# Kernel optimization log

Hardware: AMD Instinct MI355X
Metric: run time of the kernel (lower is better)

Reference implementation:

```python
import jax, jax.numpy as jnp
from jax import lax
import numpy as np

V, D, H, CO = 50000, 300, 512, 100
B, S, W = 64, 32, 128


def setup_inputs() -> dict:
    key = jax.random.key(0)
    ks = jax.random.split(key, 24)
    sc = 0.1  # mimic uniform(-0.1, 0.1)-style small init; keeps tanh unsaturated
    inp = {
        "paragraphs": jax.random.randint(ks[0], (B, S, W), 0, V, dtype=jnp.int64),
        "embed_table": jax.random.normal(ks[1], (V, D), jnp.float32),
        "conv_w3": jax.random.normal(ks[2], (CO, 1, 3, D), jnp.float32) * 0.05,
        "conv_b3": jax.random.normal(ks[3], (CO,), jnp.float32) * sc,
        "conv_w4": jax.random.normal(ks[4], (CO, 1, 4, D), jnp.float32) * 0.05,
        "conv_b4": jax.random.normal(ks[5], (CO,), jnp.float32) * sc,
        "conv_w5": jax.random.normal(ks[6], (CO, 1, 5, D), jnp.float32) * 0.05,
        "conv_b5": jax.random.normal(ks[7], (CO,), jnp.float32) * sc,
        "proj_w": jax.random.normal(ks[8], (300, 300), jnp.float32) * sc,
        "proj_b": jax.random.normal(ks[9], (300,), jnp.float32) * sc,
        "init_w": jax.random.normal(ks[10], (H, 300), jnp.float32) * sc,
        "init_b": jax.random.normal(ks[11], (H,), jnp.float32) * sc,
        "w_ih_f": jax.random.normal(ks[12], (H, 300), jnp.float32) * sc,
        "w_hh_f": jax.random.normal(ks[13], (H, H), jnp.float32) * sc,
        "b_ih_f": jax.random.normal(ks[14], (H,), jnp.float32) * sc,
        "b_hh_f": jax.random.normal(ks[15], (H,), jnp.float32) * sc,
        "w_ih_b": jax.random.normal(ks[16], (H, 300), jnp.float32) * sc,
        "w_hh_b": jax.random.normal(ks[17], (H, H), jnp.float32) * sc,
        "b_ih_b": jax.random.normal(ks[18], (H,), jnp.float32) * sc,
        "b_hh_b": jax.random.normal(ks[19], (H,), jnp.float32) * sc,
        "cls_w": jax.random.normal(ks[20], (5, 2 * H), jnp.float32) * sc,
        "cls_b": jax.random.normal(ks[21], (5,), jnp.float32) * sc,
    }
    return inp


def _cnn_text(tok, embed_table, conv_params):
    # tok: (N, W) int ids -> (N, 3*CO) sentence features (dropout = eval identity)
    emb = embed_table[tok]              # (N, W, D)
    x = emb[:, None, :, :]              # (N, 1, W, D)
    feats = []
    for w, b in conv_params:
        y = lax.conv_general_dilated(
            x, w, window_strides=(1, 1), padding="VALID",
            dimension_numbers=("NCHW", "OIHW", "NCHW"))  # (N, CO, W-K+1, 1)
        y = jax.nn.relu(y[..., 0] + b[None, :, None])       # (N, CO, W-K+1)
        feats.append(jnp.max(y, axis=2))                    # (N, CO) max-pool over time
    return jnp.concatenate(feats, axis=1)                    # (N, 3*CO)


def reference(paragraphs, embed_table, conv_w3, conv_b3, conv_w4, conv_b4,
              conv_w5, conv_b5, proj_w, proj_b, init_w, init_b,
              w_ih_f, w_hh_f, b_ih_f, b_hh_f, w_ih_b, w_hh_b, b_ih_b, b_hh_b,
              cls_w, cls_b):
    b_, s_, w_ = paragraphs.shape
    tok = paragraphs.reshape(b_ * s_, w_)
    conv_params = [(conv_w3, conv_b3), (conv_w4, conv_b4), (conv_w5, conv_b5)]
    sent = _cnn_text(tok, embed_table, conv_params).reshape(b_, s_, 3 * CO)

    # init_rnn: same init hidden for both directions
    h0 = sent[:, 0, :] @ init_w.T + init_b  # (B, H)

    def step(carry, x_t):
        hf, hb = carry
        xi = x_t @ proj_w.T + proj_b  # (B, 300)
        hf_n = jnp.tanh(xi @ w_ih_f.T + b_ih_f + hf @ w_hh_f.T + b_hh_f)
        hb_n = jnp.tanh(xi @ w_ih_b.T + b_ih_b + hb @ w_hh_b.T + b_hh_b)
        pred = jnp.concatenate([hf_n, hb_n], axis=1) @ cls_w.T + cls_b  # (B, 5)
        return (hf_n, hb_n), pred

    _, preds = lax.scan(step, (h0, h0), jnp.swapaxes(sent, 0, 1))  # (S, B, 5)
    return jnp.swapaxes(preds, 0, 1)  # (B, S, 5)
```

## Files before the change

kernel.cpp:

```cpp
#include <hip/hip_runtime.h>


#define LDSK     304
#define LDSROWB  608
#define LDSBYTES 80384

typedef __bf16   bf16x8 __attribute__((ext_vector_type(8)));
typedef float    f32x16 __attribute__((ext_vector_type(16)));
typedef _Float16 h2v    __attribute__((ext_vector_type(2)));

__global__ void prep_convw(const float* __restrict__ w3, const float* __restrict__ w4,
                           const float* __restrict__ w5, __bf16* __restrict__ Aw32) {
  int idx = blockIdx.x * 256 + threadIdx.x;
  if (idx >= 48 * 20 * 64 * 8) return;
  int i    = idx & 7;
  int lane = (idx >> 3) & 63;
  int rem  = idx >> 9;
  int ks   = rem % 20, g = rem / 20;
  int kc, cg, j; const float* w;
  if (g < 12)      { kc = 3; cg = g / 3;        j = g % 3;        w = w3; }
  else if (g < 28) { kc = 4; cg = (g - 12) / 4; j = (g - 12) % 4; w = w4; }
  else             { kc = 5; cg = (g - 28) / 5; j = (g - 28) % 5; w = w5; }
  int ch = cg * 32 + (lane & 31);
  int k  = ks * 16 + (lane >> 5) * 8 + i;
  float v = 0.f;
  if (ch < 100 && k < 300) v = w[(ch * kc + j) * 300 + k];
  Aw32[idx] = (__bf16)v;
}

__device__ __forceinline__ unsigned int packf16(float a, float b) {
  h2v h; h[0] = (_Float16)a; h[1] = (_Float16)b;
  return __builtin_bit_cast(unsigned int, h);
}
__global__ void prep_whh(const float* __restrict__ whf, const float* __restrict__ whb,
                         uint4* __restrict__ Wq) {
  int idx = blockIdx.x * 256 + threadIdx.x;
  if (idx >= 2 * 128 * 256) return;
  int dir = idx >> 15;
  int rem = idx & 32767;
  int kq = rem >> 8, tid = rem & 255;
  const float* W = dir ? whb : whf;
  const float* r0 = W + (size_t)tid * 512 + 4 * kq;
  const float* r1 = W + (size_t)(tid + 256) * 512 + 4 * kq;
  uint4 o;
  o.x = packf16(r0[0], r0[1]);
  o.y = packf16(r1[0], r1[1]);
  o.z = packf16(r0[2], r0[3]);
  o.w = packf16(r1[2], r1[3]);
  Wq[idx] = o;
}

__device__ __forceinline__ void conv_chunk32(const char* ldsc, const __bf16* __restrict__ Aw32,
                                             int GB, int kc, int cg0,
                                             const float* __restrict__ bias,
                                             int colbase, int pmax,
                                             float* __restrict__ srow, int lane) {
  const int m32 = lane & 31, hi = lane >> 5;
  f32x16 acc[2][4];
#pragma unroll
  for (int i = 0; i < 2; ++i)
#pragma unroll
    for (int n = 0; n < 4; ++n)
#pragma unroll
      for (int e = 0; e < 16; ++e) acc[i][n][e] = 0.f;

  for (int j = 0; j < kc; ++j) {
    const int row0 = m32 + j;
    const int mask = (row0 & 7) << 4;
    const int rowbyte = row0 * LDSROWB + hi * 16;
    const __bf16* a0 = Aw32 + ((size_t)((GB + cg0 * kc + j) * 20) << 9) + lane * 8;
    const __bf16* a1 = Aw32 + ((size_t)((GB + (cg0 + 1) * kc + j) * 20) << 9) + lane * 8;
#pragma unroll 2
    for (int ks = 0; ks < 20; ++ks) {
      bf16x8 bf[4];
#pragma unroll
      for (int nt = 0; nt < 4; ++nt) {
        int addr = rowbyte + nt * (32 * LDSROWB) + ks * 32;
        bf[nt] = *(const bf16x8*)(ldsc + (addr ^ mask));
      }
      bf16x8 af0 = *(const bf16x8*)(a0 + (ks << 9));
      bf16x8 af1 = *(const bf16x8*)(a1 + (ks << 9));
#pragma unroll
      for (int nt = 0; nt < 4; ++nt)
        acc[0][nt] = __builtin_amdgcn_mfma_f32_32x32x16_bf16(af0, bf[nt], acc[0][nt], 0, 0, 0);
#pragma unroll
      for (int nt = 0; nt < 4; ++nt)
        acc[1][nt] = __builtin_amdgcn_mfma_f32_32x32x16_bf16(af1, bf[nt], acc[1][nt], 0, 0, 0);
    }
  }
#pragma unroll
  for (int i = 0; i < 2; ++i) {
    float m[16];
#pragma unroll
    for (int r = 0; r < 16; ++r) m[r] = -3.0e38f;
#pragma unroll
    for (int nt = 0; nt < 4; ++nt) {
      int p = nt * 32 + m32;
      bool valid = (p <= pmax);
#pragma unroll
      for (int r = 0; r < 16; ++r)
        m[r] = fmaxf(m[r], valid ? acc[i][nt][r] : -3.0e38f);
    }
#pragma unroll
    for (int r = 0; r < 16; ++r) {
#pragma unroll
      for (int d = 1; d < 32; d <<= 1) m[r] = fmaxf(m[r], __shfl_xor(m[r], d, 64));
    }
    if (m32 == 0) {
#pragma unroll
      for (int r = 0; r < 16; ++r) {
        int ch = (cg0 + i) * 32 + (r & 3) + 8 * (r >> 2) + 4 * hi;
        if (ch < 100) srow[colbase + ch] = fmaxf(m[r] + bias[ch], 0.f);
      }
    }
  }
}

__global__ void __launch_bounds__(256, 2)
conv_kernel(const int* __restrict__ tok, const float* __restrict__ emb,
            const __bf16* __restrict__ Aw32,
            const float* __restrict__ b3, const float* __restrict__ b4, const float* __restrict__ b5,
            float* __restrict__ sent) {
  extern __shared__ __bf16 lds[];
  char* ldsc = (char*)lds;
  const int sid = blockIdx.x, tid = threadIdx.x;
  for (int i = tid; i < LDSBYTES / 4; i += 256) ((unsigned int*)lds)[i] = 0u;
  __syncthreads();
  const int* t0 = tok + sid * 128;
  for (int i = tid; i < 128 * 75; i += 256) {
    int r = i / 75, q = i - r * 75;
    long tk = (long)t0[r];
    float4 v = *(const float4*)(emb + tk * 300L + q * 4);
    union { __bf16 h[4]; uint2 u; } pk;
    pk.h[0] = (__bf16)v.x; pk.h[1] = (__bf16)v.y; pk.h[2] = (__bf16)v.z; pk.h[3] = (__bf16)v.w;
    int wb = (r * LDSROWB + q * 8) ^ ((r & 7) << 4);
    *(uint2*)(ldsc + wb) = pk.u;
  }
  __syncthreads();
  const int wave = tid >> 6, lane = tid & 63;
  float* srow = sent + (size_t)sid * 304;
  switch (wave) {
    case 0:
      conv_chunk32(ldsc, Aw32, 28, 5, 0, b5, 200, 123, srow, lane);
      break;
    case 1:
      conv_chunk32(ldsc, Aw32, 28, 5, 2, b5, 200, 123, srow, lane);
      break;
    case 2:
      conv_chunk32(ldsc, Aw32, 12, 4, 0, b4, 100, 124, srow, lane);
      conv_chunk32(ldsc, Aw32,  0, 3, 0, b3,   0, 125, srow, lane);
      break;
    default:
      conv_chunk32(ldsc, Aw32, 12, 4, 2, b4, 100, 124, srow, lane);
      conv_chunk32(ldsc, Aw32,  0, 3, 2, b3,   0, 125, srow, lane);
      break;
  }
}

__global__ void xigh0_kernel(const float* __restrict__ sent,
                             const float* __restrict__ pw, const float* __restrict__ pb,
                             const float* __restrict__ wf, const float* __restrict__ wb,
                             const float* __restrict__ bif, const float* __restrict__ bhf,
                             const float* __restrict__ bib, const float* __restrict__ bhb,
                             const float* __restrict__ iw, const float* __restrict__ ib,
                             float* __restrict__ G, float* __restrict__ h0) {
  __shared__ float s[8][300];
  __shared__ float xi[8][304];
  const int tid = threadIdx.x;
  if (blockIdx.x < 256) {
    const int rb = blockIdx.x * 8;
    for (int i = tid; i < 8 * 300; i += 256) {
      int r = i / 300, c = i - r * 300;
      s[r][c] = sent[(size_t)(rb + r) * 304 + c];
    }
    __syncthreads();
    for (int o = tid; o < 300; o += 256) {
      const float* w = pw + o * 300;
      float bvv = pb[o];
      float a[8];
#pragma unroll
      for (int r = 0; r < 8; ++r) a[r] = bvv;
      for (int k = 0; k < 300; k += 4) {
        float4 wv = *(const float4*)(w + k);
#pragma unroll
        for (int r = 0; r < 8; ++r)
          a[r] += wv.x * s[r][k] + wv.y * s[r][k + 1] + wv.z * s[r][k + 2] + wv.w * s[r][k + 3];
      }
#pragma unroll
      for (int r = 0; r < 8; ++r) xi[r][o] = a[r];
    }
    __syncthreads();
    for (int o = tid; o < 1024; o += 256) {
      int dir = o >> 9, oo = o & 511;
      const float* w = (dir ? wb : wf) + oo * 300;
      float bvv = dir ? (bib[oo] + bhb[oo]) : (bif[oo] + bhf[oo]);
      float a[8];
#pragma unroll
      for (int r = 0; r < 8; ++r) a[r] = bvv;
      for (int k = 0; k < 300; k += 4) {
        float4 wv = *(const float4*)(w + k);
#pragma unroll
        for (int r = 0; r < 8; ++r)
          a[r] += wv.x * xi[r][k] + wv.y * xi[r][k + 1] + wv.z * xi[r][k + 2] + wv.w * xi[r][k + 3];
      }
#pragma unroll
      for (int r = 0; r < 8; ++r) G[(rb + r) * 1024 + o] = a[r];
    }
  } else {
    const int bb = (blockIdx.x - 256) * 8;
    for (int i = tid; i < 8 * 300; i += 256) {
      int r = i / 300, c = i - r * 300;
      s[r][c] = sent[(size_t)((bb + r) * 32) * 304 + c];
    }
    __syncthreads();
    for (int o = tid; o < 512; o += 256) {
      const float* w = iw + o * 300;
      float bvv = ib[o];
      float a[8];
#pragma unroll
      for (int r = 0; r < 8; ++r) a[r] = bvv;
      for (int k = 0; k < 300; k += 4) {
        float4 wv = *(const float4*)(w + k);
#pragma unroll
        for (int r = 0; r < 8; ++r)
          a[r] += wv.x * s[r][k] + wv.y * s[r][k + 1] + wv.z * s[r][k + 2] + wv.w * s[r][k + 3];
      }
#pragma unroll
      for (int r = 0; r < 8; ++r) h0[(bb + r) * 512 + o] = a[r];
    }
  }
}

#if __has_builtin(__builtin_amdgcn_fdot2)
#define FDOT2(a, b, c) __builtin_amdgcn_fdot2((a), (b), (c), false)
#else
static __device__ __forceinline__ float FDOT2(h2v a, h2v b, float c) {
  return c + (float)a[0] * (float)b[0] + (float)a[1] * (float)b[1];
}
#endif
__device__ __forceinline__ h2v as_h2(unsigned int u) { return __builtin_bit_cast(h2v, u); }

__global__ void __launch_bounds__(256)
rnn_kernel(const uint4* __restrict__ Wq, const float* __restrict__ G,
           const float* __restrict__ h0, float* __restrict__ H) {
  const int blk = blockIdx.x, tid = threadIdx.x;
  const int dir = blk >> 6, b = blk & 63;
  __shared__ float hs[512];
  __shared__ uint2 h2p[128];
  for (int i = tid; i < 512; i += 256) hs[i] = h0[b * 512 + i];
  __syncthreads();
  const uint4* W = Wq + (size_t)dir * (128 * 256);
  for (int t = 0; t < 32; ++t) {
    { h2v hh; hh[0] = (_Float16)hs[2 * tid]; hh[1] = (_Float16)hs[2 * tid + 1];
      ((unsigned int*)h2p)[tid] = __builtin_bit_cast(unsigned int, hh); }
    __syncthreads();
    const float* g = G + ((size_t)(b * 32 + t)) * 1024 + dir * 512;
    float s0[4], s1[4];
    s0[0] = g[tid]; s1[0] = g[tid + 256];
    s0[1] = s0[2] = s0[3] = 0.f;
    s1[1] = s1[2] = s1[3] = 0.f;
#pragma unroll 2
    for (int kb = 0; kb < 32; ++kb) {
#pragma unroll
      for (int u = 0; u < 4; ++u) {
        int kq = kb * 4 + u;
        uint4 wv = W[kq * 256 + tid];
        uint2 hp = h2p[kq];
        h2v p = as_h2(hp.x), q = as_h2(hp.y);
        s0[u] = FDOT2(as_h2(wv.x), p, s0[u]);
        s1[u] = FDOT2(as_h2(wv.y), p, s1[u]);
        s0[u] = FDOT2(as_h2(wv.z), q, s0[u]);
        s1[u] = FDOT2(as_h2(wv.w), q, s1[u]);
      }
    }
    float a0 = (s0[0] + s0[1]) + (s0[2] + s0[3]);
    float a1 = (s1[0] + s1[1]) + (s1[2] + s1[3]);
    __syncthreads();
    float n0 = tanhf(a0), n1 = tanhf(a1);
    hs[tid] = n0; hs[tid + 256] = n1;
    float* Ht = H + ((size_t)((dir * 64 + b) * 32 + t)) * 512;
    Ht[tid] = n0; Ht[tid + 256] = n1;
    __syncthreads();
  }
}

__global__ void pred_kernel(const float* __restrict__ H, const float* __restrict__ cw,
                            const float* __restrict__ cb, float* __restrict__ out) {
  const int bt = blockIdx.x;
  const int lane = threadIdx.x;
  const int b = bt >> 5, t = bt & 31;
  const float* hf = H + ((size_t)(b * 32 + t)) * 512;
  const float* hb = H + ((size_t)((64 + b) * 32 + t)) * 512;
  for (int c = 0; c < 5; ++c) {
    const float* w = cw + c * 1024;
    float a = 0.f;
    for (int o = lane; o < 512; o += 64) a += w[o] * hf[o] + w[512 + o] * hb[o];
#pragma unroll
    for (int d = 32; d; d >>= 1) a += __shfl_down(a, d, 64);
    if (lane == 0) out[bt * 5 + c] = a + cb[c];
  }
}

extern "C" void kernel_launch(void* const* d_in, const int* in_sizes, int n_in,
                              void* d_out, int out_size, void* d_ws, size_t ws_size,
                              hipStream_t stream) {
  const int*   tok  = (const int*)d_in[0];
  const float* emb  = (const float*)d_in[1];
  const float* w3   = (const float*)d_in[2];
  const float* b3   = (const float*)d_in[3];
  const float* w4   = (const float*)d_in[4];
  const float* b4   = (const float*)d_in[5];
  const float* w5   = (const float*)d_in[6];
  const float* b5   = (const float*)d_in[7];
  const float* pw   = (const float*)d_in[8];
  const float* pb   = (const float*)d_in[9];
  const float* iw   = (const float*)d_in[10];
  const float* ib   = (const float*)d_in[11];
  const float* wihf = (const float*)d_in[12];
  const float* whhf = (const float*)d_in[13];
  const float* bihf = (const float*)d_in[14];
  const float* bhhf = (const float*)d_in[15];
  const float* wihb = (const float*)d_in[16];
  const float* whhb = (const float*)d_in[17];
  const float* bihb = (const float*)d_in[18];
  const float* bhhb = (const float*)d_in[19];
  const float* cw   = (const float*)d_in[20];
  const float* cb   = (const float*)d_in[21];
  float* out = (float*)d_out;

  char* ws = (char*)d_ws;
  __bf16* Aw32  = (__bf16*)(ws);
  uint4* Wq     = (uint4*)(ws +  1u * 1024 * 1024);
  float* sent   = (float*)(ws +  2u * 1024 * 1024);
  float* G      = (float*)(ws +  8u * 1024 * 1024);
  float* h0     = (float*)(ws + 16u * 1024 * 1024);
  float* H      = (float*)(ws + 17u * 1024 * 1024);

  prep_convw<<<1920, 256, 0, stream>>>(w3, w4, w5, Aw32);
  prep_whh<<<256, 256, 0, stream>>>(whhf, whhb, Wq);

  hipFuncSetAttribute(reinterpret_cast<const void*>(conv_kernel),
                      hipFuncAttributeMaxDynamicSharedMemorySize, LDSBYTES);
  conv_kernel<<<2048, 256, LDSBYTES, stream>>>(tok, emb, Aw32, b3, b4, b5, sent);

  xigh0_kernel<<<264, 256, 0, stream>>>(sent, pw, pb, wihf, wihb, bihf, bhhf, bihb, bhhb,
                                        iw, ib, G, h0);
  rnn_kernel<<<128, 256, 0, stream>>>(Wq, G, h0, H);
  pred_kernel<<<2048, 64, 0, stream>>>(H, cw, cb, out);
}
```

Before: 642.3 us.

## Double-buffer conv MFMA operands, trim K steps, widen RNN to 512 threads

The conv inner loop is rewritten to software-pipeline its operands: the LDS and global fragment loads for the next K step are issued before the MFMAs of the current step run. The K dimension drops from 20 to 19 steps of 16 (304 covers 300), which shrinks the packed weights and the LDS allocation. The RNN kernel moves to 512 threads with one output per thread and a matching uint2 fp16 weight layout, giving more parallelism per recurrence step. The cost is higher register pressure from double buffering, and possible LDS or padding edge issues with the reduced K extent.

New measurement: 696.2 us. 8.4% more time.

```diff
diff --git a/kernel.cpp b/kernel.cpp
--- a/kernel.cpp
+++ b/kernel.cpp
@@ -3,20 +3,22 @@
 
 #define LDSK     304
 #define LDSROWB  608
-#define LDSBYTES 80384
+#define LDSBYTES 80256
 
 typedef __bf16   bf16x8 __attribute__((ext_vector_type(8)));
 typedef float    f32x16 __attribute__((ext_vector_type(16)));
 typedef _Float16 h2v    __attribute__((ext_vector_type(2)));
 
+#define MFMA32(a, b, c) __builtin_amdgcn_mfma_f32_32x32x16_bf16((a), (b), (c), 0, 0, 0)
+
 __global__ void prep_convw(const float* __restrict__ w3, const float* __restrict__ w4,
                            const float* __restrict__ w5, __bf16* __restrict__ Aw32) {
   int idx = blockIdx.x * 256 + threadIdx.x;
-  if (idx >= 48 * 20 * 64 * 8) return;
+  if (idx >= 48 * 19 * 64 * 8) return;
   int i    = idx & 7;
   int lane = (idx >> 3) & 63;
   int rem  = idx >> 9;
-  int ks   = rem % 20, g = rem / 20;
+  int ks   = rem % 19, g = rem / 19;
   int kc, cg, j; const float* w;
   if (g < 12)      { kc = 3; cg = g / 3;        j = g % 3;        w = w3; }
   else if (g < 28) { kc = 4; cg = (g - 12) / 4; j = (g - 12) % 4; w = w4; }
@@ -33,21 +35,18 @@
   return __builtin_bit_cast(unsigned int, h);
 }
 __global__ void prep_whh(const float* __restrict__ whf, const float* __restrict__ whb,
-                         uint4* __restrict__ Wq) {
+                         uint2* __restrict__ Wq2) {
   int idx = blockIdx.x * 256 + threadIdx.x;
-  if (idx >= 2 * 128 * 256) return;
-  int dir = idx >> 15;
-  int rem = idx & 32767;
-  int kq = rem >> 8, tid = rem & 255;
+  if (idx >= 2 * 128 * 512) return;
+  int dir = idx >> 16;
+  int rem = idx & 65535;
+  int kq = rem >> 9, o = rem & 511;
   const float* W = dir ? whb : whf;
-  const float* r0 = W + (size_t)tid * 512 + 4 * kq;
-  const float* r1 = W + (size_t)(tid + 256) * 512 + 4 * kq;
-  uint4 o;
-  o.x = packf16(r0[0], r0[1]);
-  o.y = packf16(r1[0], r1[1]);
-  o.z = packf16(r0[2], r0[3]);
-  o.w = packf16(r1[2], r1[3]);
-  Wq[idx] = o;
+  const float* r0 = W + (size_t)o * 512 + 4 * kq;
+  uint2 v;
+  v.x = packf16(r0[0], r0[1]);
+  v.y = packf16(r0[2], r0[3]);
+  Wq2[idx] = v;
 }
 
 __device__ __forceinline__ void conv_chunk32(const char* ldsc, const __bf16* __restrict__ Aw32,
@@ -68,25 +67,41 @@
     const int row0 = m32 + j;
     const int mask = (row0 & 7) << 4;
     const int rowbyte = row0 * LDSROWB + hi * 16;
-    const __bf16* a0 = Aw32 + ((size_t)((GB + cg0 * kc + j) * 20) << 9) + lane * 8;
-    const __bf16* a1 = Aw32 + ((size_t)((GB + (cg0 + 1) * kc + j) * 20) << 9) + lane * 8;
-#pragma unroll 2
-    for (int ks = 0; ks < 20; ++ks) {
-      bf16x8 bf[4];
-#pragma unroll
-      for (int nt = 0; nt < 4; ++nt) {
-        int addr = rowbyte + nt * (32 * LDSROWB) + ks * 32;
-        bf[nt] = *(const bf16x8*)(ldsc + (addr ^ mask));
-      }
-      bf16x8 af0 = *(const bf16x8*)(a0 + (ks << 9));
-      bf16x8 af1 = *(const bf16x8*)(a1 + (ks << 9));
+    const __bf16* a0 = Aw32 + (size_t)(GB + cg0 * kc + j) * (19 * 512) + lane * 8;
+    const __bf16* a1 = Aw32 + (size_t)(GB + (cg0 + 1) * kc + j) * (19 * 512) + lane * 8;
+
+    bf16x8 bA[4], bB[4], aA0, aA1, aB0, aB1;
+#pragma unroll
+    for (int nt = 0; nt < 4; ++nt)
+      bA[nt] = *(const bf16x8*)(ldsc + ((rowbyte + nt * (32 * LDSROWB)) ^ mask));
+    aA0 = *(const bf16x8*)(a0);
+    aA1 = *(const bf16x8*)(a1);
+#pragma unroll
+    for (int kp = 0; kp < 9; ++kp) {
+      const int ksB = 2 * kp + 1, ksA = 2 * kp + 2;
 #pragma unroll
       for (int nt = 0; nt < 4; ++nt)
-        acc[0][nt] = __builtin_amdgcn_mfma_f32_32x32x16_bf16(af0, bf[nt], acc[0][nt], 0, 0, 0);
+        bB[nt] = *(const bf16x8*)(ldsc + ((rowbyte + nt * (32 * LDSROWB) + ksB * 32) ^ mask));
+      aB0 = *(const bf16x8*)(a0 + ksB * 512);
+      aB1 = *(const bf16x8*)(a1 + ksB * 512);
+#pragma unroll
+      for (int nt = 0; nt < 4; ++nt) acc[0][nt] = MFMA32(aA0, bA[nt], acc[0][nt]);
+#pragma unroll
+      for (int nt = 0; nt < 4; ++nt) acc[1][nt] = MFMA32(aA1, bA[nt], acc[1][nt]);
 #pragma unroll
       for (int nt = 0; nt < 4; ++nt)
-        acc[1][nt] = __builtin_amdgcn_mfma_f32_32x32x16_bf16(af1, bf[nt], acc[1][nt], 0, 0, 0);
-    }
+        bA[nt] = *(const bf16x8*)(ldsc + ((rowbyte + nt * (32 * LDSROWB) + ksA * 32) ^ mask));
+      aA0 = *(const bf16x8*)(a0 + ksA * 512);
+      aA1 = *(const bf16x8*)(a1 + ksA * 512);
+#pragma unroll
+      for (int nt = 0; nt < 4; ++nt) acc[0][nt] = MFMA32(aB0, bB[nt], acc[0][nt]);
+#pragma unroll
+      for (int nt = 0; nt < 4; ++nt) acc[1][nt] = MFMA32(aB1, bB[nt], acc[1][nt]);
+    }
+#pragma unroll
+    for (int nt = 0; nt < 4; ++nt) acc[0][nt] = MFMA32(aA0, bA[nt], acc[0][nt]);
+#pragma unroll
+    for (int nt = 0; nt < 4; ++nt) acc[1][nt] = MFMA32(aA1, bA[nt], acc[1][nt]);
   }
 #pragma unroll
   for (int i = 0; i < 2; ++i) {
@@ -240,46 +255,39 @@
 #endif
 __device__ __forceinline__ h2v as_h2(unsigned int u) { return __builtin_bit_cast(h2v, u); }
 
-__global__ void __launch_bounds__(256)
-rnn_kernel(const uint4* __restrict__ Wq, const float* __restrict__ G,
+__global__ void __launch_bounds__(512)
+rnn_kernel(const uint2* __restrict__ Wq2, const float* __restrict__ G,
            const float* __restrict__ h0, float* __restrict__ H) {
   const int blk = blockIdx.x, tid = threadIdx.x;
   const int dir = blk >> 6, b = blk & 63;
   __shared__ float hs[512];
   __shared__ uint2 h2p[128];
-  for (int i = tid; i < 512; i += 256) hs[i] = h0[b * 512 + i];
+  hs[tid] = h0[b * 512 + tid];
   __syncthreads();
-  const uint4* W = Wq + (size_t)dir * (128 * 256);
+  const uint2* W = Wq2 + (size_t)dir * (128 * 512);
   for (int t = 0; t < 32; ++t) {
-    { h2v hh; hh[0] = (_Float16)hs[2 * tid]; hh[1] = (_Float16)hs[2 * tid + 1];
-      ((unsigned int*)h2p)[tid] = __builtin_bit_cast(unsigned int, hh); }
-    __syncthreads();
-    const float* g = G + ((size_t)(b * 32 + t)) * 1024 + dir * 512;
-    float s0[4], s1[4];
-    s0[0] = g[tid]; s1[0] = g[tid + 256];
-    s0[1] = s0[2] = s0[3] = 0.f;
-    s1[1] = s1[2] = s1[3] = 0.f;
-#pragma unroll 2
+    if (tid < 256) {
+      ((unsigned int*)h2p)[tid] = packf16(hs[2 * tid], hs[2 * tid + 1]);
+    }
+    __syncthreads();
+    const float* g = G + (size_t)(b * 32 + t) * 1024 + dir * 512;
+    float s0 = g[tid], s1 = 0.f, s2 = 0.f, s3 = 0.f;
+#pragma unroll 4
     for (int kb = 0; kb < 32; ++kb) {
-#pragma unroll
-      for (int u = 0; u < 4; ++u) {
-        int kq = kb * 4 + u;
-        uint4 wv = W[kq * 256 + tid];
-        uint2 hp = h2p[kq];
-        h2v p = as_h2(hp.x), q = as_h2(hp.y);
-        s0[u] = FDOT2(as_h2(wv.x), p, s0[u]);
-        s1[u] = FDOT2(as_h2(wv.y), p, s1[u]);
-        s0[u] = FDOT2(as_h2(wv.z), q, s0[u]);
-        s1[u] = FDOT2(as_h2(wv.w), q, s1[u]);
-      }
-    }
-    float a0 = (s0[0] + s0[1]) + (s0[2] + s0[3]);
-    float a1 = (s1[0] + s1[1]) + (s1[2] + s1[3]);
-    __syncthreads();
-    float n0 = tanhf(a0), n1 = tanhf(a1);
-    hs[tid] = n0; hs[tid + 256] = n1;
-    float* Ht = H + ((size_t)((dir * 64 + b) * 32 + t)) * 512;
-    Ht[tid] = n0; Ht[tid + 256] = n1;
+      int kq = kb * 4;
+      uint2 w0 = W[(kq + 0) * 512 + tid]; uint2 p0 = h2p[kq + 0];
+      uint2 w1 = W[(kq + 1) * 512 + tid]; uint2 p1 = h2p[kq + 1];
+      uint2 w2 = W[(kq + 2) * 512 + tid]; uint2 p2 = h2p[kq + 2];
+      uint2 w3 = W[(kq + 3) * 512 + tid]; uint2 p3 = h2p[kq + 3];
+      s0 = FDOT2(as_h2(w0.x), as_h2(p0.x), s0); s0 = FDOT2(as_h2(w0.y), as_h2(p0.y), s0);
+      s1 = FDOT2(as_h2(w1.x), as_h2(p1.x), s1); s1 = FDOT2(as_h2(w1.y), as_h2(p1.y), s1);
+      s2 = FDOT2(as_h2(w2.x), as_h2(p2.x), s2); s2 = FDOT2(as_h2(w2.y), as_h2(p2.y), s2);
+      s3 = FDOT2(as_h2(w3.x), as_h2(p3.x), s3); s3 = FDOT2(as_h2(w3.y), as_h2(p3.y), s3);
+    }
+    float n = tanhf((s0 + s1) + (s2 + s3));
+    __syncthreads();
+    hs[tid] = n;
+    H[(size_t)((dir * 64 + b) * 32 + t) * 512 + tid] = n;
     __syncthreads();
   }
 }
@@ -330,14 +338,14 @@
 
   char* ws = (char*)d_ws;
   __bf16* Aw32  = (__bf16*)(ws);
-  uint4* Wq     = (uint4*)(ws +  1u * 1024 * 1024);
+  uint2* Wq2    = (uint2*)(ws +  1u * 1024 * 1024);
   float* sent   = (float*)(ws +  2u * 1024 * 1024);
   float* G      = (float*)(ws +  8u * 1024 * 1024);
   float* h0     = (float*)(ws + 16u * 1024 * 1024);
   float* H      = (float*)(ws + 17u * 1024 * 1024);
 
-  prep_convw<<<1920, 256, 0, stream>>>(w3, w4, w5, Aw32);
-  prep_whh<<<256, 256, 0, stream>>>(whhf, whhb, Wq);
+  prep_convw<<<1824, 256, 0, stream>>>(w3, w4, w5, Aw32);
+  prep_whh<<<512, 256, 0, stream>>>(whhf, whhb, Wq2);
 
   hipFuncSetAttribute(reinterpret_cast<const void*>(conv_kernel),
                       hipFuncAttributeMaxDynamicSharedMemorySize, LDSBYTES);
@@ -345,6 +353,6 @@
 
   xigh0_kernel<<<264, 256, 0, stream>>>(sent, pw, pb, wihf, wihb, bihf, bhhf, bihb, bhhb,
                                         iw, ib, G, h0);
-  rnn_kernel<<<128, 256, 0, stream>>>(Wq, G, h0, H);
+  rnn_kernel<<<128, 512, 0, stream>>>(Wq2, G, h0, H);
   pred_kernel<<<2048, 64, 0, stream>>>(H, cw, cb, out);
 }
```
